# Optimization experiments

Hardware: AMD Instinct MI355X
Metric: run time of the kernel (lower is better)

The kernel has to match this reference:

```python
import jax, jax.numpy as jnp
import numpy as np

EPS = 1e-5

def _layernorm(x, gamma, beta):
    # LayerNormalization over last axis (channels), epsilon=1e-5
    mu = jnp.mean(x, axis=-1, keepdims=True)
    var = jnp.var(x, axis=-1, keepdims=True)
    return (x - mu) * jax.lax.rsqrt(var + EPS) * gamma + beta

def setup_inputs() -> dict:
    key = jax.random.key(0)
    ks = jax.random.split(key, 6)
    B, H, W, C = 8, 64, 64, 256
    std = 0.1  # NIN init_scale
    return {
        "x": jax.random.normal(ks[0], (B, H, W, C), dtype=jnp.float32),
        "ln_gamma": jnp.ones((C,), dtype=jnp.float32),
        "ln_beta": jnp.zeros((C,), dtype=jnp.float32),
        "wq": jax.random.normal(ks[1], (C, C), dtype=jnp.float32) * std,
        "bq": jnp.zeros((C,), dtype=jnp.float32),
        "wk": jax.random.normal(ks[2], (C, C), dtype=jnp.float32) * std,
        "bk": jnp.zeros((C,), dtype=jnp.float32),
        "wv": jax.random.normal(ks[3], (C, C), dtype=jnp.float32) * std,
        "bv": jnp.zeros((C,), dtype=jnp.float32),
        "wo": jax.random.normal(ks[4], (C, C), dtype=jnp.float32) * std,
        "bo": jnp.zeros((C,), dtype=jnp.float32),
    }

def reference(x, ln_gamma, ln_beta, wq, bq, wk, bk, wv, bv, wo, bo):
    B, H, W, C = x.shape
    h = _layernorm(x, ln_gamma, ln_beta)
    # 1x1 convs == per-pixel channel matmuls
    q = jnp.einsum('bhwc,cd->bhwd', h, wq) + bq
    k = jnp.einsum('bhwc,cd->bhwd', h, wk) + bk
    v = jnp.einsum('bhwc,cd->bhwd', h, wv) + bv
    scale = jnp.float32(C) ** -0.5
    # dense spatial attention over all H*W tokens
    w = jnp.einsum('bhwc,bijc->bhwij', q, k) * scale  # [B,H,W,H,W]
    w = jax.nn.softmax(w.reshape(B, H, W, H * W), axis=-1).reshape(B, H, W, H, W)
    h = jnp.einsum('bhwij,bijc->bhwc', w, v)
    h = jnp.einsum('bhwc,cd->bhwd', h, wo) + bo
    return x + h
```

## Files before the change

kernel.cpp:

```cpp
#include <hip/hip_runtime.h>
#include <stdint.h>

#define NB    8
#define NTOK  4096
#define TOK   32768
#define CDIM  256
#define BQ    128
#define BK    64
#define NT    (NTOK / BK)

#define KPITCH 264
#define VPITCH 68
#define KTILE_SH (BK * KPITCH)
#define VTILE_SH (CDIM * VPITCH)
#define KCH   33
#define VCH   34
#define TOTCH (KCH + VCH)

typedef __attribute__((ext_vector_type(8))) short bf16x8;
typedef __attribute__((ext_vector_type(4))) float f32x4;

#define SSCALE 0.09016844f

static __device__ __forceinline__ unsigned short f2bf(float f) {
    union { float f; unsigned u; } v; v.f = f;
    unsigned r = v.u + 0x7fffu + ((v.u >> 16) & 1u);
    return (unsigned short)(r >> 16);
}

static __device__ __forceinline__ void dma16(const unsigned short* g, unsigned short* l) {
    __builtin_amdgcn_global_load_lds(
        (const __attribute__((address_space(1))) unsigned int*)g,
        (__attribute__((address_space(3))) unsigned int*)l,
        16, 0, 0);
}

__global__ __launch_bounds__(256) void wtrans_kernel(
        const float* __restrict__ w0, const float* __restrict__ w1,
        const float* __restrict__ w2, const float* __restrict__ w3,
        unsigned short* __restrict__ wt) {
    int id = blockIdx.x;
    int m = id >> 8, dd = id & 255;
    const float* src = (m == 0) ? w0 : (m == 1) ? w1 : (m == 2) ? w2 : w3;
    wt[m * (CDIM * CDIM) + dd * CDIM + threadIdx.x] = f2bf(src[threadIdx.x * CDIM + dd]);
}

__global__ __launch_bounds__(128) void qkv_kernel(
        const float* __restrict__ x,
        const float* __restrict__ gamma,
        const float* __restrict__ beta,
        const unsigned short* __restrict__ wts,
        const float* __restrict__ bq,
        const float* __restrict__ bk,
        const float* __restrict__ bv,
        unsigned short* __restrict__ q_bf,
        unsigned short* __restrict__ k2,
        unsigned short* __restrict__ vt2) {
    __shared__ unsigned short VT[64][VPITCH];
    int tid = threadIdx.x;
    int w = tid >> 6, lane = tid & 63, quad = lane >> 4, l16 = lane & 15;
    int blk = blockIdx.x;
    int gy = blockIdx.y;
    int nt0 = gy * 4;
    int tok_base = blk * 64 + w * 32;

    bf16x8 afr[2][8];
    #pragma unroll
    for (int s = 0; s < 2; ++s) {
        const float* xr = x + (size_t)(tok_base + s * 16 + l16) * CDIM;
        float s1 = 0.f, s2 = 0.f;
        #pragma unroll
        for (int kk = 0; kk < 8; ++kk) {
            float4 a = *(const float4*)(xr + kk * 32 + quad * 8);
            float4 c = *(const float4*)(xr + kk * 32 + quad * 8 + 4);
            s1 += a.x + a.y + a.z + a.w + c.x + c.y + c.z + c.w;
            s2 += a.x * a.x + a.y * a.y + a.z * a.z + a.w * a.w
                + c.x * c.x + c.y * c.y + c.z * c.z + c.w * c.w;
        }
        s1 += __shfl_xor(s1, 16, 64); s1 += __shfl_xor(s1, 32, 64);
        s2 += __shfl_xor(s2, 16, 64); s2 += __shfl_xor(s2, 32, 64);
        float mean = s1 * (1.0f / 256.0f);
        float var  = s2 * (1.0f / 256.0f) - mean * mean;
        float rstd = rsqrtf(var + 1e-5f);
        #pragma unroll
        for (int kk = 0; kk < 8; ++kk) {
            float4 a  = *(const float4*)(xr + kk * 32 + quad * 8);
            float4 c  = *(const float4*)(xr + kk * 32 + quad * 8 + 4);
            float4 g0 = *(const float4*)(gamma + kk * 32 + quad * 8);
            float4 g1 = *(const float4*)(gamma + kk * 32 + quad * 8 + 4);
            float4 b0 = *(const float4*)(beta + kk * 32 + quad * 8);
            float4 b1 = *(const float4*)(beta + kk * 32 + quad * 8 + 4);
            union { bf16x8 v; unsigned short u[8]; } pk;
            pk.u[0] = f2bf((a.x - mean) * rstd * g0.x + b0.x);
            pk.u[1] = f2bf((a.y - mean) * rstd * g0.y + b0.y);
            pk.u[2] = f2bf((a.z - mean) * rstd * g0.z + b0.z);
            pk.u[3] = f2bf((a.w - mean) * rstd * g0.w + b0.w);
            pk.u[4] = f2bf((c.x - mean) * rstd * g1.x + b1.x);
            pk.u[5] = f2bf((c.y - mean) * rstd * g1.y + b1.y);
            pk.u[6] = f2bf((c.z - mean) * rstd * g1.z + b1.z);
            pk.u[7] = f2bf((c.w - mean) * rstd * g1.w + b1.w);
            afr[s][kk] = pk.v;
        }
    }

    {
        const unsigned short* wq_t = wts;
        #pragma unroll
        for (int ntl = 0; ntl < 4; ++ntl) {
            int nt = nt0 + ntl;
            f32x4 acc0 = {0.f, 0.f, 0.f, 0.f};
            f32x4 acc1 = {0.f, 0.f, 0.f, 0.f};
            #pragma unroll
            for (int kk = 0; kk < 8; ++kk) {
                bf16x8 bfr = *(const bf16x8*)(wq_t + (size_t)(nt * 16 + l16) * CDIM + kk * 32 + quad * 8);
                acc0 = __builtin_amdgcn_mfma_f32_16x16x32_bf16(bfr, afr[0][kk], acc0, 0, 0, 0);
                acc1 = __builtin_amdgcn_mfma_f32_16x16x32_bf16(bfr, afr[1][kk], acc1, 0, 0, 0);
            }
            int d0 = nt * 16 + quad * 4;
            float4 b4 = *(const float4*)(bq + d0);
            ushort4 o0, o1;
            o0.x = f2bf((acc0[0] + b4.x) * SSCALE); o0.y = f2bf((acc0[1] + b4.y) * SSCALE);
            o0.z = f2bf((acc0[2] + b4.z) * SSCALE); o0.w = f2bf((acc0[3] + b4.w) * SSCALE);
            o1.x = f2bf((acc1[0] + b4.x) * SSCALE); o1.y = f2bf((acc1[1] + b4.y) * SSCALE);
            o1.z = f2bf((acc1[2] + b4.z) * SSCALE); o1.w = f2bf((acc1[3] + b4.w) * SSCALE);
            *(ushort4*)(q_bf + (size_t)(tok_base + l16) * CDIM + d0)      = o0;
            *(ushort4*)(q_bf + (size_t)(tok_base + 16 + l16) * CDIM + d0) = o1;
        }
    }
    {
        const unsigned short* wk_t = wts + CDIM * CDIM;
        unsigned short* kdst = k2 + (size_t)blk * KTILE_SH;
        int key0 = w * 32 + l16;
        #pragma unroll
        for (int ntl = 0; ntl < 4; ++ntl) {
            int nt = nt0 + ntl;
            f32x4 acc0 = {0.f, 0.f, 0.f, 0.f};
            f32x4 acc1 = {0.f, 0.f, 0.f, 0.f};
            #pragma unroll
            for (int kk = 0; kk < 8; ++kk) {
                bf16x8 bfr = *(const bf16x8*)(wk_t + (size_t)(nt * 16 + l16) * CDIM + kk * 32 + quad * 8);
                acc0 = __builtin_amdgcn_mfma_f32_16x16x32_bf16(bfr, afr[0][kk], acc0, 0, 0, 0);
                acc1 = __builtin_amdgcn_mfma_f32_16x16x32_bf16(bfr, afr[1][kk], acc1, 0, 0, 0);
            }
            int d0 = nt * 16 + quad * 4;
            float4 b4 = *(const float4*)(bk + d0);
            ushort4 o0, o1;
            o0.x = f2bf(acc0[0] + b4.x); o0.y = f2bf(acc0[1] + b4.y);
            o0.z = f2bf(acc0[2] + b4.z); o0.w = f2bf(acc0[3] + b4.w);
            o1.x = f2bf(acc1[0] + b4.x); o1.y = f2bf(acc1[1] + b4.y);
            o1.z = f2bf(acc1[2] + b4.z); o1.w = f2bf(acc1[3] + b4.w);
            *(ushort4*)(kdst + (size_t)key0 * KPITCH + d0)        = o0;
            *(ushort4*)(kdst + (size_t)(key0 + 16) * KPITCH + d0) = o1;
        }
    }
    {
        const unsigned short* wv_t = wts + 2 * CDIM * CDIM;
        #pragma unroll
        for (int ntl = 0; ntl < 4; ++ntl) {
            int nt = nt0 + ntl;
            f32x4 acc0 = {0.f, 0.f, 0.f, 0.f};
            f32x4 acc1 = {0.f, 0.f, 0.f, 0.f};
            #pragma unroll
            for (int kk = 0; kk < 8; ++kk) {
                bf16x8 bfr = *(const bf16x8*)(wv_t + (size_t)(nt * 16 + l16) * CDIM + kk * 32 + quad * 8);
                acc0 = __builtin_amdgcn_mfma_f32_16x16x32_bf16(afr[0][kk], bfr, acc0, 0, 0, 0);
                acc1 = __builtin_amdgcn_mfma_f32_16x16x32_bf16(afr[1][kk], bfr, acc1, 0, 0, 0);
            }
            int d = nt * 16 + l16;
            float bb = bv[d];
            int dl = ntl * 16 + l16;
            #pragma unroll
            for (int r = 0; r < 4; ++r) {
                VT[dl][w * 32 + quad * 8 + r]     = f2bf(acc0[r] + bb);
                VT[dl][w * 32 + quad * 8 + 4 + r] = f2bf(acc1[r] + bb);
            }
        }
    }
    __syncthreads();
    const uint4* src = (const uint4*)(&VT[0][0]);
    uint4* dst = (uint4*)(vt2 + (size_t)blk * VTILE_SH + (size_t)gy * 64 * VPITCH);
    #pragma unroll
    for (int i = 0; i < 4; ++i)
        dst[i * 128 + tid] = src[i * 128 + tid];
    if (tid < 32) dst[512 + tid] = src[512 + tid];
}

#define DMA_TILE(KS, VS, ktn)                                                        \
    {                                                                                \
        const unsigned short* gk = k2 + (size_t)(b * NT + (ktn)) * KTILE_SH;         \
        const unsigned short* gv = vt2 + (size_t)(b * NT + (ktn)) * VTILE_SH;        \
        for (int c = w; c < TOTCH; c += 8) {                                         \
            if (c < KCH) dma16(gk + c * 512 + lane * 8, &KS[0][0] + c * 512);        \
            else dma16(gv + (c - KCH) * 512 + lane * 8, &VS[0][0] + (c - KCH) * 512);\
        }                                                                            \
    }

#define COMPUTE_TILE(KS, VS)                                                         \
    {                                                                                \
        f32x4 sfr[2][2];                                                             \
        __builtin_amdgcn_s_setprio(1);                                               \
        _Pragma("unroll")                                                            \
        for (int nt = 0; nt < 2; ++nt) {                                             \
            f32x4 a0 = {0.f, 0.f, 0.f, 0.f};                                         \
            f32x4 a1 = {0.f, 0.f, 0.f, 0.f};                                         \
            _Pragma("unroll")                                                        \
            for (int kk = 0; kk < 8; ++kk) {                                         \
                bf16x8 kb = *(const bf16x8*)(&KS[kh * 32 + nt * 16 + l16][kk * 32 + quad * 8]); \
                a0 = __builtin_amdgcn_mfma_f32_16x16x32_bf16(kb, qfr[0][kk], a0, 0, 0, 0);      \
                a1 = __builtin_amdgcn_mfma_f32_16x16x32_bf16(kb, qfr[1][kk], a1, 0, 0, 0);      \
            }                                                                        \
            sfr[0][nt] = a0; sfr[1][nt] = a1;                                        \
        }                                                                            \
        __builtin_amdgcn_s_setprio(0);                                               \
        int4 pwv[2];                                                                 \
        _Pragma("unroll")                                                            \
        for (int s = 0; s < 2; ++s) {                                                \
            unsigned pw[4];                                                          \
            _Pragma("unroll")                                                        \
            for (int nt = 0; nt < 2; ++nt)                                           \
                _Pragma("unroll")                                                    \
                for (int h = 0; h < 2; ++h) {                                        \
                    float plo = exp2f(sfr[s][nt][2 * h]);                            \
                    float phi = exp2f(sfr[s][nt][2 * h + 1]);                        \
                    lacc[s] += plo + phi;                                            \
                    pw[nt * 2 + h] = (__float_as_uint(plo) >> 16)                    \
                                   | (__float_as_uint(phi) & 0xffff0000u);           \
                }                                                                    \
            pwv[s] = make_int4(pw[0], pw[1], pw[2], pw[3]);                          \
        }                                                                            \
        bf16x8 pfr0 = *(bf16x8*)&pwv[0];                                             \
        bf16x8 pfr1 = *(bf16x8*)&pwv[1];                                             \
        __builtin_amdgcn_s_setprio(1);                                               \
        _Pragma("unroll")                                                            \
        for (int nt2 = 0; nt2 < 16; ++nt2) {                                         \
            bf16x8 vb = *(const bf16x8*)(&VS[nt2 * 16 + l16][kh * 32 + quad * 8]);   \
            O[0][nt2] = __builtin_amdgcn_mfma_f32_16x16x32_bf16(pfr0, vb, O[0][nt2], 0, 0, 0);  \
            O[1][nt2] = __builtin_amdgcn_mfma_f32_16x16x32_bf16(pfr1, vb, O[1][nt2], 0, 0, 0);  \
        }                                                                            \
        __builtin_amdgcn_s_setprio(0);                                               \
    }

__global__ __launch_bounds__(512, 2) void flash_kernel(
        const unsigned short* __restrict__ q_bf,
        const unsigned short* __restrict__ k2,
        const unsigned short* __restrict__ vt2,
        const unsigned short* __restrict__ wo_t,
        const float* __restrict__ bo,
        const float* __restrict__ x,
        float* __restrict__ out) {
    __shared__ unsigned short Ks0[BK][KPITCH];
    __shared__ unsigned short Ks1[BK][KPITCH];
    __shared__ unsigned short Vs0[CDIM][VPITCH];
    __shared__ unsigned short Vs1[CDIM][VPITCH];
    __shared__ float sLbuf[512];

    int tid = threadIdx.x;
    int w = tid >> 6, lane = tid & 63, quad = lane >> 4, l16 = lane & 15;
    int kh = w >> 2;
    int wq = w & 3;
    int bid = blockIdx.x;
    int b = bid & 7;
    int qtile = bid >> 3;
    int qrow = qtile * BQ + wq * 32;
    const size_t bbase = (size_t)b * NTOK * CDIM;

    bf16x8 qfr[2][8];
    #pragma unroll
    for (int s = 0; s < 2; ++s)
        #pragma unroll
        for (int kk = 0; kk < 8; ++kk)
            qfr[s][kk] = *(const bf16x8*)(q_bf + bbase + (size_t)(qrow + s * 16 + l16) * CDIM + kk * 32 + quad * 8);

    f32x4 O[2][16];
    #pragma unroll
    for (int s = 0; s < 2; ++s)
        #pragma unroll
        for (int i = 0; i < 16; ++i) O[s][i] = (f32x4){0.f, 0.f, 0.f, 0.f};
    float lacc[2] = {0.f, 0.f};

    DMA_TILE(Ks0, Vs0, 0);
    __syncthreads();

    for (int kt2 = 0; kt2 < NT; kt2 += 2) {
        DMA_TILE(Ks1, Vs1, kt2 + 1);
        COMPUTE_TILE(Ks0, Vs0);
        __syncthreads();
        if (kt2 + 2 < NT) DMA_TILE(Ks0, Vs0, kt2 + 2);
        COMPUTE_TILE(Ks1, Vs1);
        __syncthreads();
    }

    float* sO = (wq == 0) ? (float*)&Ks0[0][0] : (wq == 1) ? (float*)&Ks1[0][0]
              : (wq == 2) ? (float*)&Vs0[0][0] : (float*)&Vs1[0][0];
    float* sL = sLbuf + wq * 128;

    if (kh == 1) {
        #pragma unroll
        for (int s = 0; s < 2; ++s) {
            #pragma unroll
            for (int nt2 = 0; nt2 < 16; ++nt2)
                #pragma unroll
                for (int r = 0; r < 4; ++r)
                    sO[((s * 16 + nt2) * 4 + r) * 64 + lane] = O[s][nt2][r];
            sL[s * 64 + lane] = lacc[s];
        }
    }
    __syncthreads();
    if (kh == 0) {
        float lr[2][4];
        #pragma unroll
        for (int s = 0; s < 2; ++s) {
            float ls = lacc[s] + sL[s * 64 + lane];
            ls += __shfl_xor(ls, 16, 64);
            ls += __shfl_xor(ls, 32, 64);
            float li = 1.0f / ls;
            #pragma unroll
            for (int r = 0; r < 4; ++r)
                lr[s][r] = __shfl(li, quad * 4 + r, 64);
        }
        #pragma unroll
        for (int s = 0; s < 2; ++s)
            #pragma unroll
            for (int nt2 = 0; nt2 < 16; ++nt2)
                #pragma unroll
                for (int r = 0; r < 4; ++r)
                    O[s][nt2][r] = (O[s][nt2][r] + sO[((s * 16 + nt2) * 4 + r) * 64 + lane]) * lr[s][r];
    }
    __syncthreads();

    if (kh == 0) {
        if (wq < 2) {
            #pragma unroll
            for (int s = 0; s < 2; ++s)
                #pragma unroll
                for (int nt2 = 0; nt2 < 16; ++nt2)
                    #pragma unroll
                    for (int r = 0; r < 4; ++r)
                        Ks0[(wq & 1) * 32 + s * 16 + quad * 4 + r][nt2 * 16 + l16] = f2bf(O[s][nt2][r]);
        } else {
            #pragma unroll
            for (int s = 0; s < 2; ++s)
                #pragma unroll
                for (int nt2 = 0; nt2 < 16; ++nt2)
                    #pragma unroll
                    for (int r = 0; r < 4; ++r)
                        Ks1[(wq & 1) * 32 + s * 16 + quad * 4 + r][nt2 * 16 + l16] = f2bf(O[s][nt2][r]);
        }
    }
    __syncthreads();

    {
        bf16x8 wfr[2][8];
        #pragma unroll
        for (int t = 0; t < 2; ++t)
            #pragma unroll
            for (int kk = 0; kk < 8; ++kk)
                wfr[t][kk] = *(const bf16x8*)(wo_t + (size_t)((w * 2 + t) * 16 + l16) * CDIM + kk * 32 + quad * 8);
        float bb0 = bo[(w * 2 + 0) * 16 + l16];
        float bb1 = bo[(w * 2 + 1) * 16 + l16];
        int tok0 = qtile * BQ;
        #pragma unroll
        for (int rg = 0; rg < 8; ++rg) {
            bf16x8 afr2[8];
            #pragma unroll
            for (int kk = 0; kk < 8; ++kk)
                afr2[kk] = (rg < 4)
                    ? *(const bf16x8*)(&Ks0[rg * 16 + l16][kk * 32 + quad * 8])
                    : *(const bf16x8*)(&Ks1[(rg - 4) * 16 + l16][kk * 32 + quad * 8]);
            f32x4 acc0 = {0.f, 0.f, 0.f, 0.f};
            f32x4 acc1 = {0.f, 0.f, 0.f, 0.f};
            #pragma unroll
            for (int kk = 0; kk < 8; ++kk) {
                acc0 = __builtin_amdgcn_mfma_f32_16x16x32_bf16(afr2[kk], wfr[0][kk], acc0, 0, 0, 0);
                acc1 = __builtin_amdgcn_mfma_f32_16x16x32_bf16(afr2[kk], wfr[1][kk], acc1, 0, 0, 0);
            }
            #pragma unroll
            for (int r = 0; r < 4; ++r) {
                size_t idx = bbase + (size_t)(tok0 + rg * 16 + quad * 4 + r) * CDIM;
                size_t i0 = idx + (w * 2 + 0) * 16 + l16;
                size_t i1 = idx + (w * 2 + 1) * 16 + l16;
                out[i0] = x[i0] + acc0[r] + bb0;
                out[i1] = x[i1] + acc1[r] + bb1;
            }
        }
    }
}

extern "C" void kernel_launch(void* const* d_in, const int* in_sizes, int n_in,
                              void* d_out, int out_size, void* d_ws, size_t ws_size,
                              hipStream_t stream) {
    const float* x     = (const float*)d_in[0];
    const float* gamma = (const float*)d_in[1];
    const float* beta  = (const float*)d_in[2];
    const float* wq    = (const float*)d_in[3];
    const float* bq    = (const float*)d_in[4];
    const float* wk    = (const float*)d_in[5];
    const float* bk    = (const float*)d_in[6];
    const float* wv    = (const float*)d_in[7];
    const float* bv    = (const float*)d_in[8];
    const float* wo    = (const float*)d_in[9];
    const float* bo    = (const float*)d_in[10];
    float* out = (float*)d_out;

    char* ws = (char*)d_ws;
    unsigned short* q_bf = (unsigned short*)(ws + 16777216);
    unsigned short* k2   = (unsigned short*)(ws + 33554432);
    unsigned short* vt2  = (unsigned short*)(ws + 50855936);
    unsigned short* wt   = (unsigned short*)(ws + 68681728);

    wtrans_kernel<<<1024, 256, 0, stream>>>(wq, wk, wv, wo, wt);
    qkv_kernel<<<dim3(TOK / 64, 4), 128, 0, stream>>>(x, gamma, beta, wt, bq, bk, bv, q_bf, k2, vt2);
    flash_kernel<<<(NTOK / BQ) * NB, 512, 0, stream>>>(
        q_bf, k2, vt2, wt + 3 * (CDIM * CDIM), bo, x, out);
}
```

Before: 375.3 us.

## Compute LayerNorm once per token block and share via LDS across QKV waves

The QKV projection kernel previously ran a 4-way grid over output-column groups, so each token's LayerNorm was recomputed four times and x was re-read repeatedly. The new kernel gives each 256-thread block 32 tokens: it normalizes them once with coalesced row loads, stores the bf16 result in shared memory, and each of the four waves handles a different column group. The V transpose staging is remapped to match. This trades redundant global reads and LN math for an extra LDS round trip and a barrier.

```diff
diff --git a/kernel.cpp b/kernel.cpp
--- a/kernel.cpp
+++ b/kernel.cpp
@@ -45,7 +45,7 @@
     wt[m * (CDIM * CDIM) + dd * CDIM + threadIdx.x] = f2bf(src[threadIdx.x * CDIM + dd]);
 }
 
-__global__ __launch_bounds__(128) void qkv_kernel(
+__global__ __launch_bounds__(256, 4) void lnqkv_kernel(
         const float* __restrict__ x,
         const float* __restrict__ gamma,
         const float* __restrict__ beta,
@@ -56,52 +56,62 @@
         unsigned short* __restrict__ q_bf,
         unsigned short* __restrict__ k2,
         unsigned short* __restrict__ vt2) {
-    __shared__ unsigned short VT[64][VPITCH];
+    __shared__ unsigned short HT[32][KPITCH];
+    __shared__ unsigned short VT[256][36];
     int tid = threadIdx.x;
     int w = tid >> 6, lane = tid & 63, quad = lane >> 4, l16 = lane & 15;
     int blk = blockIdx.x;
-    int gy = blockIdx.y;
-    int nt0 = gy * 4;
-    int tok_base = blk * 64 + w * 32;
-
-    bf16x8 afr[2][8];
-    #pragma unroll
-    for (int s = 0; s < 2; ++s) {
-        const float* xr = x + (size_t)(tok_base + s * 16 + l16) * CDIM;
+    int tok_base = blk * 32;
+    int nt0 = w * 4;
+
+    {
+        int t_loc = w * 8 + (lane >> 3);
+        int cg = (lane & 7) * 32;
+        const float* xr = x + (size_t)(tok_base + t_loc) * CDIM + cg;
         float s1 = 0.f, s2 = 0.f;
-        #pragma unroll
-        for (int kk = 0; kk < 8; ++kk) {
-            float4 a = *(const float4*)(xr + kk * 32 + quad * 8);
-            float4 c = *(const float4*)(xr + kk * 32 + quad * 8 + 4);
-            s1 += a.x + a.y + a.z + a.w + c.x + c.y + c.z + c.w;
-            s2 += a.x * a.x + a.y * a.y + a.z * a.z + a.w * a.w
-                + c.x * c.x + c.y * c.y + c.z * c.z + c.w * c.w;
-        }
-        s1 += __shfl_xor(s1, 16, 64); s1 += __shfl_xor(s1, 32, 64);
-        s2 += __shfl_xor(s2, 16, 64); s2 += __shfl_xor(s2, 32, 64);
+        float4 xv[8];
+        #pragma unroll
+        for (int j = 0; j < 8; ++j) {
+            xv[j] = ((const float4*)xr)[j];
+            s1 += xv[j].x + xv[j].y + xv[j].z + xv[j].w;
+            s2 += xv[j].x * xv[j].x + xv[j].y * xv[j].y
+                + xv[j].z * xv[j].z + xv[j].w * xv[j].w;
+        }
+        #pragma unroll
+        for (int off = 1; off < 8; off <<= 1) {
+            s1 += __shfl_xor(s1, off, 64);
+            s2 += __shfl_xor(s2, off, 64);
+        }
         float mean = s1 * (1.0f / 256.0f);
         float var  = s2 * (1.0f / 256.0f) - mean * mean;
         float rstd = rsqrtf(var + 1e-5f);
         #pragma unroll
-        for (int kk = 0; kk < 8; ++kk) {
-            float4 a  = *(const float4*)(xr + kk * 32 + quad * 8);
-            float4 c  = *(const float4*)(xr + kk * 32 + quad * 8 + 4);
-            float4 g0 = *(const float4*)(gamma + kk * 32 + quad * 8);
-            float4 g1 = *(const float4*)(gamma + kk * 32 + quad * 8 + 4);
-            float4 b0 = *(const float4*)(beta + kk * 32 + quad * 8);
-            float4 b1 = *(const float4*)(beta + kk * 32 + quad * 8 + 4);
-            union { bf16x8 v; unsigned short u[8]; } pk;
-            pk.u[0] = f2bf((a.x - mean) * rstd * g0.x + b0.x);
-            pk.u[1] = f2bf((a.y - mean) * rstd * g0.y + b0.y);
-            pk.u[2] = f2bf((a.z - mean) * rstd * g0.z + b0.z);
-            pk.u[3] = f2bf((a.w - mean) * rstd * g0.w + b0.w);
-            pk.u[4] = f2bf((c.x - mean) * rstd * g1.x + b1.x);
-            pk.u[5] = f2bf((c.y - mean) * rstd * g1.y + b1.y);
-            pk.u[6] = f2bf((c.z - mean) * rstd * g1.z + b1.z);
-            pk.u[7] = f2bf((c.w - mean) * rstd * g1.w + b1.w);
-            afr[s][kk] = pk.v;
-        }
-    }
+        for (int j = 0; j < 8; j += 2) {
+            float4 xa = xv[j], xb = xv[j + 1];
+            float4 ga = ((const float4*)(gamma + cg))[j];
+            float4 gb = ((const float4*)(gamma + cg))[j + 1];
+            float4 ba = ((const float4*)(beta + cg))[j];
+            float4 bb4 = ((const float4*)(beta + cg))[j + 1];
+            union { uint4 u; unsigned short us[8]; } pk;
+            pk.us[0] = f2bf((xa.x - mean) * rstd * ga.x + ba.x);
+            pk.us[1] = f2bf((xa.y - mean) * rstd * ga.y + ba.y);
+            pk.us[2] = f2bf((xa.z - mean) * rstd * ga.z + ba.z);
+            pk.us[3] = f2bf((xa.w - mean) * rstd * ga.w + ba.w);
+            pk.us[4] = f2bf((xb.x - mean) * rstd * gb.x + bb4.x);
+            pk.us[5] = f2bf((xb.y - mean) * rstd * gb.y + bb4.y);
+            pk.us[6] = f2bf((xb.z - mean) * rstd * gb.z + bb4.z);
+            pk.us[7] = f2bf((xb.w - mean) * rstd * gb.w + bb4.w);
+            *(uint4*)(&HT[t_loc][cg + j * 4]) = pk.u;
+        }
+    }
+    __syncthreads();
+
+    bf16x8 afr[2][8];
+    #pragma unroll
+    for (int s = 0; s < 2; ++s)
+        #pragma unroll
+        for (int kk = 0; kk < 8; ++kk)
+            afr[s][kk] = *(const bf16x8*)(&HT[s * 16 + l16][kk * 32 + quad * 8]);
 
     {
         const unsigned short* wq_t = wts;
@@ -129,8 +139,8 @@
     }
     {
         const unsigned short* wk_t = wts + CDIM * CDIM;
-        unsigned short* kdst = k2 + (size_t)blk * KTILE_SH;
-        int key0 = w * 32 + l16;
+        unsigned short* kdst = k2 + (size_t)(blk >> 1) * KTILE_SH;
+        int key0 = (blk & 1) * 32 + l16;
         #pragma unroll
         for (int ntl = 0; ntl < 4; ++ntl) {
             int nt = nt0 + ntl;
@@ -168,21 +178,23 @@
             }
             int d = nt * 16 + l16;
             float bb = bv[d];
-            int dl = ntl * 16 + l16;
             #pragma unroll
             for (int r = 0; r < 4; ++r) {
-                VT[dl][w * 32 + quad * 8 + r]     = f2bf(acc0[r] + bb);
-                VT[dl][w * 32 + quad * 8 + 4 + r] = f2bf(acc1[r] + bb);
-            }
-        }
-    }
-    __syncthreads();
-    const uint4* src = (const uint4*)(&VT[0][0]);
-    uint4* dst = (uint4*)(vt2 + (size_t)blk * VTILE_SH + (size_t)gy * 64 * VPITCH);
-    #pragma unroll
-    for (int i = 0; i < 4; ++i)
-        dst[i * 128 + tid] = src[i * 128 + tid];
-    if (tid < 32) dst[512 + tid] = src[512 + tid];
+                VT[d][quad * 8 + r]     = f2bf(acc0[r] + bb);
+                VT[d][quad * 8 + 4 + r] = f2bf(acc1[r] + bb);
+            }
+        }
+    }
+    __syncthreads();
+    {
+        unsigned short* vdst = vt2 + (size_t)(blk >> 1) * VTILE_SH + (blk & 1) * 32;
+        #pragma unroll
+        for (int i = 0; i < 4; ++i) {
+            int idx = i * 256 + tid;
+            int row = idx >> 2, c = idx & 3;
+            *(uint4*)(vdst + (size_t)row * VPITCH + c * 8) = *(const uint4*)(&VT[row][c * 8]);
+        }
+    }
 }
 
 #define DMA_TILE(KS, VS, ktn)                                                        \
@@ -409,7 +421,7 @@
     unsigned short* wt   = (unsigned short*)(ws + 68681728);
 
     wtrans_kernel<<<1024, 256, 0, stream>>>(wq, wk, wv, wo, wt);
-    qkv_kernel<<<dim3(TOK / 64, 4), 128, 0, stream>>>(x, gamma, beta, wt, bq, bk, bv, q_bf, k2, vt2);
+    lnqkv_kernel<<<1024, 256, 0, stream>>>(x, gamma, beta, wt, bq, bk, bv, q_bf, k2, vt2);
     flash_kernel<<<(NTOK / BQ) * NB, 512, 0, stream>>>(
         q_bf, k2, vt2, wt + 3 * (CDIM * CDIM), bo, x, out);
 }
```

Result: faster. 330.0 us (-12.1%).
